# Kernel optimization log

Measured on AMD Instinct MI355X. Metric: run time of the kernel, lower is better.

Reference implementation:

```python
import jax, jax.numpy as jnp
import numpy as np

B, C = 4096, 128
EPS_BN = 1e-5  # torch BatchNorm1d default eps
EPS_ATT = 1e-9


def setup_inputs() -> dict:
    key = jax.random.key(0)
    ks = jax.random.split(key, 6)
    x1 = jax.random.normal(ks[0], (B, C, 1), jnp.float32)
    x2 = jax.random.normal(ks[1], (B, C, 1), jnp.float32)
    x1_2 = jax.random.normal(ks[2], (B, C, 1), jnp.float32)
    # trans_conv: Conv1d(C, C, kernel_size=1) -> weight (C_out, C_in)
    conv_w = jax.random.normal(ks[3], (C, C), jnp.float32) / np.sqrt(C).astype(np.float32)
    conv_b = jnp.zeros((C,), jnp.float32)
    # BatchNorm1d(C) affine params
    bn_gamma = jnp.ones((C,), jnp.float32)
    bn_beta = jnp.zeros((C,), jnp.float32)
    # fc_relation: Linear(2C+1, 1)
    fc_w = jax.random.normal(ks[4], (1, 2 * C + 1), jnp.float32) / np.sqrt(2 * C + 1).astype(np.float32)
    fc_b = jnp.zeros((1,), jnp.float32)
    return {"x1": x1, "x2": x2, "x1_2": x1_2, "conv_w": conv_w, "conv_b": conv_b,
            "bn_gamma": bn_gamma, "bn_beta": bn_beta, "fc_w": fc_w, "fc_b": fc_b}


def reference(x1, x2, x1_2, conv_w, conv_b, bn_gamma, bn_beta, fc_w, fc_b):
    # energy = bmm(x1, x2^T): (B,C,1) x (B,1,C) -> (B,C,C) outer product
    energy = jnp.einsum('bcl,bdl->bcd', x1, x2)
    energy = jax.nn.softmax(energy, axis=-1)
    # normalize columns (sum over dim=1)
    attention = energy / (EPS_ATT + energy.sum(axis=1, keepdims=True))
    # x_r = bmm(attention, x1_2): (B,C,C) x (B,C,1) -> (B,C,1)
    x_r = jnp.einsum('bcd,bdl->bcl', attention, x1_2)
    # 1x1 conv = per-position channel mixing
    t = jnp.einsum('oc,bcl->bol', conv_w, x_r) + conv_b[None, :, None]
    y = x1 - t
    # BatchNorm1d in training mode: per-channel stats over (batch, length)
    mean = y.mean(axis=(0, 2), keepdims=True)          # (1,C,1)
    var = y.var(axis=(0, 2), keepdims=True)            # biased variance
    y = (y - mean) * jax.lax.rsqrt(var + EPS_BN)
    y = y * bn_gamma[None, :, None] + bn_beta[None, :, None]
    x_r_out = jax.nn.relu(y)                            # (B,C,1)
    # gated fusion: cat([energy, energy^T, x1], dim=2) -> (B, C, 2C+1)
    feat = jnp.concatenate([energy, jnp.swapaxes(energy, 1, 2), x1], axis=2)
    gate = jax.nn.sigmoid(jnp.einsum('bcf,of->bco', feat, fc_w) + fc_b)  # (B,C,1)
    return gate * x1 + x_r_out
```

## Files before the change

### kernel.cpp

```cpp
#include <hip/hip_runtime.h>

#define B_ 4096
#define C_ 128
#define EPS_ATT 1e-9f
#define EPS_BN 1e-5f
#define LOG2E 1.44269504088896f

using short8 = __attribute__((ext_vector_type(8))) short;
using f32x4 = __attribute__((ext_vector_type(4))) float;
using us4 = __attribute__((ext_vector_type(4))) unsigned short;
using u32x2 = __attribute__((ext_vector_type(2))) unsigned int;

__device__ __forceinline__ unsigned short bf16b(float x) {
    __bf16 h = (__bf16)x;
    return __builtin_bit_cast(unsigned short, h);
}

__global__ __launch_bounds__(256, 4) void k_batch(
    const float* __restrict__ x1, const float* __restrict__ x2,
    const float* __restrict__ x12,
    const float* __restrict__ fcw, const float* __restrict__ fcb,
    float* __restrict__ XR, float* __restrict__ GX1) {
    const int b = blockIdx.x;
    const int tid = threadIdx.x;
    const int lane = tid & 63;
    const int w = tid >> 6;
    const int g = lane >> 4;
    const int ls = lane & 15;

    __shared__ char s_buf[C_ * C_ * 2] __attribute__((aligned(16)));
    __shared__ float s_x1[C_] __attribute__((aligned(16)));
    __shared__ float s_x2[C_] __attribute__((aligned(16)));
    __shared__ float s_fcC[C_] __attribute__((aligned(16)));
    __shared__ float s_invZ[C_] __attribute__((aligned(16)));
    __shared__ float s_cs4[4][C_] __attribute__((aligned(16)));
    __shared__ float s_s24[4][C_] __attribute__((aligned(16)));
    __shared__ unsigned short s_f1bf[C_] __attribute__((aligned(16)));

    float* s_S1 = (float*)s_buf;
    float* s_xrr = (float*)(s_buf + 512);
    unsigned short* s_w3bf = (unsigned short*)(s_buf + 1024);

    float v12 = 0.f;
    if (tid < C_) {
        s_x1[tid] = x1[b * C_ + tid];
        s_x2[tid] = x2[b * C_ + tid];
        s_f1bf[tid] = bf16b(fcw[tid]);
        s_fcC[tid] = fcw[C_ + tid];
        v12 = x12[b * C_ + tid];
    }
    __syncthreads();

    short8 ef0[4], ef1[4];
    float zp0 = 0.f, zp1 = 0.f;
    {
        const float r0 = s_x1[32 * w + ls] * LOG2E;
        const float r1 = s_x1[32 * w + 16 + ls] * LOG2E;
        char* erow0 = s_buf + (32 * w + ls) * 256;
        char* erow1 = s_buf + (32 * w + 16 + ls) * 256;
        const int sw = (ls & 7) << 4;
#pragma unroll
        for (int q = 0; q < 4; ++q) {
            f32x4 xa = *(const f32x4*)&s_x2[32 * q + 8 * g];
            f32x4 xb = *(const f32x4*)&s_x2[32 * q + 8 * g + 4];
            union {
                short8 v;
                unsigned short u[8];
            } p0, p1;
#pragma unroll
            for (int j = 0; j < 4; ++j) {
                float a0 = __builtin_amdgcn_exp2f(r0 * xa[j]);
                float b0 = __builtin_amdgcn_exp2f(r0 * xb[j]);
                float a1 = __builtin_amdgcn_exp2f(r1 * xa[j]);
                float b1 = __builtin_amdgcn_exp2f(r1 * xb[j]);
                zp0 += a0 + b0;
                zp1 += a1 + b1;
                p0.u[j] = bf16b(a0);
                p0.u[j + 4] = bf16b(b0);
                p1.u[j] = bf16b(a1);
                p1.u[j + 4] = bf16b(b1);
            }
            ef0[q] = p0.v;
            ef1[q] = p1.v;
            const int off = (64 * q + 16 * g) ^ sw;
            *(short8*)(erow0 + off) = p0.v;
            *(short8*)(erow1 + off) = p1.v;
        }
    }
    zp0 += __shfl_xor(zp0, 16);
    zp0 += __shfl_xor(zp0, 32);
    zp1 += __shfl_xor(zp1, 16);
    zp1 += __shfl_xor(zp1, 32);
    if (lane < 16) {
        s_invZ[32 * w + ls] = 1.f / zp0;
        s_invZ[32 * w + 16 + ls] = 1.f / zp1;
    }
    __syncthreads();

    {
        const int grp = tid & 31;
        const int sl = tid >> 5;
        const char* eb = s_buf + sl * 16 * 256;
        const int octb = grp >> 1;
        const int hoff = (grp & 1) * 8;
        float cs[4] = {0.f, 0.f, 0.f, 0.f};
        float s2[4] = {0.f, 0.f, 0.f, 0.f};
#pragma unroll
        for (int k = 0; k < 4; ++k) {
            f32x4 iz4 = *(const f32x4*)&s_invZ[sl * 16 + 4 * k];
            f32x4 fc4 = *(const f32x4*)&s_fcC[sl * 16 + 4 * k];
#pragma unroll
            for (int rr = 0; rr < 4; ++rr) {
                const int r = 4 * k + rr;
                const float iz = iz4[rr];
                const float izf = iz * fc4[rr];
                u32x2 ev = *(const u32x2*)(eb + r * 256 +
                                           ((octb ^ (r & 7)) << 4) + hoff);
#pragma unroll
                for (int d = 0; d < 2; ++d) {
                    float elo = __builtin_bit_cast(float, ev[d] << 16);
                    float ehi =
                        __builtin_bit_cast(float, ev[d] & 0xffff0000u);
                    cs[2 * d] = fmaf(elo, iz, cs[2 * d]);
                    s2[2 * d] = fmaf(elo, izf, s2[2 * d]);
                    cs[2 * d + 1] = fmaf(ehi, iz, cs[2 * d + 1]);
                    s2[2 * d + 1] = fmaf(ehi, izf, s2[2 * d + 1]);
                }
            }
        }
#pragma unroll
        for (int k = 0; k < 4; ++k) {
            cs[k] += __shfl_xor(cs[k], 32);
            s2[k] += __shfl_xor(s2[k], 32);
        }
        if ((sl & 1) == 0) {
            f32x4 c4 = {cs[0], cs[1], cs[2], cs[3]};
            f32x4 t4 = {s2[0], s2[1], s2[2], s2[3]};
            *(f32x4*)&s_cs4[w][grp * 4] = c4;
            *(f32x4*)&s_s24[w][grp * 4] = t4;
        }
    }
    __syncthreads();

    if (tid < C_) {
        float cs = s_cs4[0][tid] + s_cs4[1][tid] + s_cs4[2][tid] + s_cs4[3][tid];
        float w3 = v12 / (EPS_ATT + cs);
        s_w3bf[tid] = bf16b(w3);
    }
    __syncthreads();

    {
        const short8 z8 = {0, 0, 0, 0, 0, 0, 0, 0};
        short8 bq[4];
#pragma unroll
        for (int q = 0; q < 4; ++q) {
            if (ls == 0)
                bq[q] = *(const short8*)&s_f1bf[q * 32 + g * 8];
            else if (ls == 1)
                bq[q] = *(const short8*)&s_w3bf[q * 32 + g * 8];
            else
                bq[q] = z8;
        }
        f32x4 acc0 = {0.f, 0.f, 0.f, 0.f};
        f32x4 acc1 = {0.f, 0.f, 0.f, 0.f};
#pragma unroll
        for (int q = 0; q < 4; ++q) {
            acc0 = __builtin_amdgcn_mfma_f32_16x16x32_bf16(ef0[q], bq[q], acc0, 0, 0, 0);
            acc1 = __builtin_amdgcn_mfma_f32_16x16x32_bf16(ef1[q], bq[q], acc1, 0, 0, 0);
        }
        if (ls < 2) {
            float* dst = ls ? s_xrr : s_S1;
            *(f32x4*)&dst[(2 * w + 0) * 16 + g * 4] = acc0;
            *(f32x4*)&dst[(2 * w + 1) * 16 + g * 4] = acc1;
        }
    }
    __syncthreads();

    if (tid < C_) {
        float invz = s_invZ[tid];
        float S1 = s_S1[tid] * invz;
        float xr = s_xrr[tid] * invz;
        float S2 = s_s24[0][tid] + s_s24[1][tid] + s_s24[2][tid] + s_s24[3][tid];
        XR[b * C_ + tid] = xr;
        float gg = S1 + S2 + s_x1[tid] * fcw[2 * C_] + fcb[0];
        float gate = 1.f / (1.f + __builtin_amdgcn_exp2f(-LOG2E * gg));
        GX1[b * C_ + tid] = gate * s_x1[tid];
    }
}

__global__ __launch_bounds__(512) void k_conv(
    const float* __restrict__ W, const float* __restrict__ XR,
    const float* __restrict__ x1, const float* __restrict__ convb,
    float* __restrict__ Y, float* __restrict__ pst) {
    const int blk = blockIdx.x;
    const int tid = threadIdx.x;
    const int bb = blk * 16;
    const int lane = tid & 63;
    const int wid = tid >> 6;
    const int g = lane >> 4;
    const int ls = lane & 15;

    __shared__ unsigned short s_Wb[C_ * C_] __attribute__((aligned(16)));
    __shared__ unsigned short s_xrb[16 * 136] __attribute__((aligned(16)));

    {
        const int r = tid >> 2;
        const int c0 = (tid & 3) * 4;
        const float* src = W + r * C_ + c0 * 8;
#pragma unroll
        for (int c = 0; c < 4; ++c) {
            f32x4 a = *(const f32x4*)(src + c * 8);
            f32x4 b2 = *(const f32x4*)(src + c * 8 + 4);
            union {
                short8 v;
                unsigned short u[8];
            } p;
#pragma unroll
            for (int j = 0; j < 4; ++j) {
                p.u[j] = bf16b(a[j]);
                p.u[j + 4] = bf16b(b2[j]);
            }
            *(short8*)&s_Wb[r * C_ + (((c0 + c) ^ (r & 7)) << 3)] = p.v;
        }
    }
    {
        const int r = tid >> 5;
        const int c = (tid & 31) * 4;
        f32x4 a = *(const f32x4*)&XR[(bb + r) * C_ + c];
        us4 p;
#pragma unroll
        for (int j = 0; j < 4; ++j) p[j] = bf16b(a[j]);
        *(us4*)&s_xrb[r * 136 + c] = p;
    }
    __syncthreads();

    {
        const int n = 16 * wid + ls;
        short8 aq[4], bq[4];
#pragma unroll
        for (int q = 0; q < 4; ++q) {
            aq[q] = *(const short8*)&s_xrb[ls * 136 + 32 * q + 8 * g];
            bq[q] = *(const short8*)&s_Wb[n * C_ + (((4 * q + g) ^ (n & 7)) << 3)];
        }
        f32x4 acc = {0.f, 0.f, 0.f, 0.f};
#pragma unroll
        for (int q = 0; q < 4; ++q)
            acc = __builtin_amdgcn_mfma_f32_16x16x32_bf16(aq[q], bq[q], acc, 0, 0, 0);

        const float cbv = convb[n];
        float ps = 0.f, pq = 0.f;
#pragma unroll
        for (int r = 0; r < 4; ++r) {
            const int m = 4 * g + r;
            float y = x1[(bb + m) * C_ + n] - (acc[r] + cbv);
            Y[(bb + m) * C_ + n] = y;
            ps += y;
            pq += y * y;
        }
        ps += __shfl_xor(ps, 16);
        ps += __shfl_xor(ps, 32);
        pq += __shfl_xor(pq, 16);
        pq += __shfl_xor(pq, 32);
        if (lane < 16) {
            pst[n * 256 + blk] = ps;
            pst[32768 + n * 256 + blk] = pq;
        }
    }
}

__global__ __launch_bounds__(256) void k_fold(const float* __restrict__ pst,
                                              const float* __restrict__ gamma,
                                              const float* __restrict__ beta,
                                              float* __restrict__ AB) {
    const int ch = blockIdx.x;
    const int t = threadIdx.x;
    __shared__ float sh[256];
    __shared__ float sh2[256];
    sh[t] = pst[ch * 256 + t];
    sh2[t] = pst[32768 + ch * 256 + t];
    __syncthreads();
    for (int off = 128; off > 0; off >>= 1) {
        if (t < off) {
            sh[t] += sh[t + off];
            sh2[t] += sh2[t + off];
        }
        __syncthreads();
    }
    if (t == 0) {
        float mean = sh[0] / (float)B_;
        float var = sh2[0] / (float)B_ - mean * mean;
        float A = gamma[ch] * rsqrtf(var + EPS_BN);
        AB[ch] = A;
        AB[C_ + ch] = beta[ch] - mean * A;
    }
}

__global__ __launch_bounds__(256) void k_final(const float* __restrict__ Y,
                                               const float* __restrict__ AB,
                                               float* __restrict__ out) {
    __shared__ float sA[C_];
    __shared__ float sB[C_];
    const int t = threadIdx.x;
    if (t < C_) {
        sA[t] = AB[t];
        sB[t] = AB[C_ + t];
    }
    __syncthreads();
    const int i4 = blockIdx.x * 256 + t;
    float4 y = ((const float4*)Y)[i4];
    float4 o = ((const float4*)out)[i4];
    const int ch = (i4 * 4) & (C_ - 1);
    o.x += fmaxf(y.x * sA[ch + 0] + sB[ch + 0], 0.f);
    o.y += fmaxf(y.y * sA[ch + 1] + sB[ch + 1], 0.f);
    o.z += fmaxf(y.z * sA[ch + 2] + sB[ch + 2], 0.f);
    o.w += fmaxf(y.w * sA[ch + 3] + sB[ch + 3], 0.f);
    ((float4*)out)[i4] = o;
}

extern "C" void kernel_launch(void* const* d_in, const int* in_sizes, int n_in,
                              void* d_out, int out_size, void* d_ws,
                              size_t ws_size, hipStream_t stream) {
    const float* x1 = (const float*)d_in[0];
    const float* x2 = (const float*)d_in[1];
    const float* x12 = (const float*)d_in[2];
    const float* convw = (const float*)d_in[3];
    const float* convb = (const float*)d_in[4];
    const float* gamma = (const float*)d_in[5];
    const float* beta = (const float*)d_in[6];
    const float* fcw = (const float*)d_in[7];
    const float* fcb = (const float*)d_in[8];
    float* out = (float*)d_out;

    float* XR = (float*)d_ws;
    float* Y = XR + (size_t)B_ * C_;
    float* pst = Y + (size_t)B_ * C_;
    float* AB = pst + 2 * C_ * 256;

    k_batch<<<B_, 256, 0, stream>>>(x1, x2, x12, fcw, fcb, XR, out);
    k_conv<<<256, 512, 0, stream>>>(convw, XR, x1, convb, Y, pst);
    k_fold<<<C_, 256, 0, stream>>>(pst, gamma, beta, AB);
    k_final<<<(B_ * C_ / 4) / 256, 256, 0, stream>>>(Y, AB, out);
}
```

Measured before the change: 35.24 us.

## Make batch kernel loop over four batches per block with register prefetch

The per-batch attention/gate kernel now launches 1024 blocks. Each block processes four batch rows in a loop instead of one row per block. The next row's x1/x2/x1_2 values are loaded into registers while the current row is computed, hiding global load latency. The fc weights and bias are loaded once per block rather than once per row. In exchange each block runs a longer serial chain, and there are fewer independent blocks for the scheduler to hide latency with.

```diff
diff --git a/kernel.cpp b/kernel.cpp
--- a/kernel.cpp
+++ b/kernel.cpp
@@ -5,6 +5,8 @@
 #define EPS_ATT 1e-9f
 #define EPS_BN 1e-5f
 #define LOG2E 1.44269504088896f
+#define GRID_KB 1024
+#define NPB 4
 
 using short8 = __attribute__((ext_vector_type(8))) short;
 using f32x4 = __attribute__((ext_vector_type(4))) float;
@@ -21,7 +23,6 @@
     const float* __restrict__ x12,
     const float* __restrict__ fcw, const float* __restrict__ fcb,
     float* __restrict__ XR, float* __restrict__ GX1) {
-    const int b = blockIdx.x;
     const int tid = threadIdx.x;
     const int lane = tid & 63;
     const int w = tid >> 6;
@@ -41,150 +42,173 @@
     float* s_xrr = (float*)(s_buf + 512);
     unsigned short* s_w3bf = (unsigned short*)(s_buf + 1024);
 
-    float v12 = 0.f;
     if (tid < C_) {
-        s_x1[tid] = x1[b * C_ + tid];
-        s_x2[tid] = x2[b * C_ + tid];
         s_f1bf[tid] = bf16b(fcw[tid]);
         s_fcC[tid] = fcw[C_ + tid];
-        v12 = x12[b * C_ + tid];
-    }
-    __syncthreads();
-
-    short8 ef0[4], ef1[4];
-    float zp0 = 0.f, zp1 = 0.f;
-    {
-        const float r0 = s_x1[32 * w + ls] * LOG2E;
-        const float r1 = s_x1[32 * w + 16 + ls] * LOG2E;
-        char* erow0 = s_buf + (32 * w + ls) * 256;
-        char* erow1 = s_buf + (32 * w + 16 + ls) * 256;
-        const int sw = (ls & 7) << 4;
-#pragma unroll
-        for (int q = 0; q < 4; ++q) {
-            f32x4 xa = *(const f32x4*)&s_x2[32 * q + 8 * g];
-            f32x4 xb = *(const f32x4*)&s_x2[32 * q + 8 * g + 4];
-            union {
-                short8 v;
-                unsigned short u[8];
-            } p0, p1;
-#pragma unroll
-            for (int j = 0; j < 4; ++j) {
-                float a0 = __builtin_amdgcn_exp2f(r0 * xa[j]);
-                float b0 = __builtin_amdgcn_exp2f(r0 * xb[j]);
-                float a1 = __builtin_amdgcn_exp2f(r1 * xa[j]);
-                float b1 = __builtin_amdgcn_exp2f(r1 * xb[j]);
-                zp0 += a0 + b0;
-                zp1 += a1 + b1;
-                p0.u[j] = bf16b(a0);
-                p0.u[j + 4] = bf16b(b0);
-                p1.u[j] = bf16b(a1);
-                p1.u[j + 4] = bf16b(b1);
-            }
-            ef0[q] = p0.v;
-            ef1[q] = p1.v;
-            const int off = (64 * q + 16 * g) ^ sw;
-            *(short8*)(erow0 + off) = p0.v;
-            *(short8*)(erow1 + off) = p1.v;
-        }
-    }
-    zp0 += __shfl_xor(zp0, 16);
-    zp0 += __shfl_xor(zp0, 32);
-    zp1 += __shfl_xor(zp1, 16);
-    zp1 += __shfl_xor(zp1, 32);
-    if (lane < 16) {
-        s_invZ[32 * w + ls] = 1.f / zp0;
-        s_invZ[32 * w + 16 + ls] = 1.f / zp1;
-    }
-    __syncthreads();
-
-    {
-        const int grp = tid & 31;
-        const int sl = tid >> 5;
-        const char* eb = s_buf + sl * 16 * 256;
-        const int octb = grp >> 1;
-        const int hoff = (grp & 1) * 8;
-        float cs[4] = {0.f, 0.f, 0.f, 0.f};
-        float s2[4] = {0.f, 0.f, 0.f, 0.f};
-#pragma unroll
-        for (int k = 0; k < 4; ++k) {
-            f32x4 iz4 = *(const f32x4*)&s_invZ[sl * 16 + 4 * k];
-            f32x4 fc4 = *(const f32x4*)&s_fcC[sl * 16 + 4 * k];
-#pragma unroll
-            for (int rr = 0; rr < 4; ++rr) {
-                const int r = 4 * k + rr;
-                const float iz = iz4[rr];
-                const float izf = iz * fc4[rr];
-                u32x2 ev = *(const u32x2*)(eb + r * 256 +
-                                           ((octb ^ (r & 7)) << 4) + hoff);
-#pragma unroll
-                for (int d = 0; d < 2; ++d) {
-                    float elo = __builtin_bit_cast(float, ev[d] << 16);
-                    float ehi =
-                        __builtin_bit_cast(float, ev[d] & 0xffff0000u);
-                    cs[2 * d] = fmaf(elo, iz, cs[2 * d]);
-                    s2[2 * d] = fmaf(elo, izf, s2[2 * d]);
-                    cs[2 * d + 1] = fmaf(ehi, iz, cs[2 * d + 1]);
-                    s2[2 * d + 1] = fmaf(ehi, izf, s2[2 * d + 1]);
+    }
+    const float fc2C = fcw[2 * C_];
+    const float fcb0 = fcb[0];
+
+    int b = blockIdx.x;
+    float pv1 = 0.f, pv2 = 0.f, pv12 = 0.f;
+    if (tid < C_) {
+        pv1 = x1[b * C_ + tid];
+        pv2 = x2[b * C_ + tid];
+        pv12 = x12[b * C_ + tid];
+    }
+
+    for (int it = 0; it < NPB; ++it, b += GRID_KB) {
+        float v12 = 0.f;
+        if (tid < C_) {
+            s_x1[tid] = pv1;
+            s_x2[tid] = pv2;
+            v12 = pv12;
+        }
+        __syncthreads();
+
+        if (it + 1 < NPB && tid < C_) {
+            pv1 = x1[(b + GRID_KB) * C_ + tid];
+            pv2 = x2[(b + GRID_KB) * C_ + tid];
+            pv12 = x12[(b + GRID_KB) * C_ + tid];
+        }
+
+        short8 ef0[4], ef1[4];
+        float zp0 = 0.f, zp1 = 0.f;
+        {
+            const float r0 = s_x1[32 * w + ls] * LOG2E;
+            const float r1 = s_x1[32 * w + 16 + ls] * LOG2E;
+            char* erow0 = s_buf + (32 * w + ls) * 256;
+            char* erow1 = s_buf + (32 * w + 16 + ls) * 256;
+            const int sw = (ls & 7) << 4;
+#pragma unroll
+            for (int q = 0; q < 4; ++q) {
+                f32x4 xa = *(const f32x4*)&s_x2[32 * q + 8 * g];
+                f32x4 xb = *(const f32x4*)&s_x2[32 * q + 8 * g + 4];
+                union {
+                    short8 v;
+                    unsigned short u[8];
+                } p0, p1;
+#pragma unroll
+                for (int j = 0; j < 4; ++j) {
+                    float a0 = __builtin_amdgcn_exp2f(r0 * xa[j]);
+                    float b0 = __builtin_amdgcn_exp2f(r0 * xb[j]);
+                    float a1 = __builtin_amdgcn_exp2f(r1 * xa[j]);
+                    float b1 = __builtin_amdgcn_exp2f(r1 * xb[j]);
+                    zp0 += a0 + b0;
+                    zp1 += a1 + b1;
+                    p0.u[j] = bf16b(a0);
+                    p0.u[j + 4] = bf16b(b0);
+                    p1.u[j] = bf16b(a1);
+                    p1.u[j + 4] = bf16b(b1);
                 }
-            }
-        }
-#pragma unroll
-        for (int k = 0; k < 4; ++k) {
-            cs[k] += __shfl_xor(cs[k], 32);
-            s2[k] += __shfl_xor(s2[k], 32);
-        }
-        if ((sl & 1) == 0) {
-            f32x4 c4 = {cs[0], cs[1], cs[2], cs[3]};
-            f32x4 t4 = {s2[0], s2[1], s2[2], s2[3]};
-            *(f32x4*)&s_cs4[w][grp * 4] = c4;
-            *(f32x4*)&s_s24[w][grp * 4] = t4;
-        }
-    }
-    __syncthreads();
-
-    if (tid < C_) {
-        float cs = s_cs4[0][tid] + s_cs4[1][tid] + s_cs4[2][tid] + s_cs4[3][tid];
-        float w3 = v12 / (EPS_ATT + cs);
-        s_w3bf[tid] = bf16b(w3);
-    }
-    __syncthreads();
-
-    {
-        const short8 z8 = {0, 0, 0, 0, 0, 0, 0, 0};
-        short8 bq[4];
-#pragma unroll
-        for (int q = 0; q < 4; ++q) {
-            if (ls == 0)
-                bq[q] = *(const short8*)&s_f1bf[q * 32 + g * 8];
-            else if (ls == 1)
-                bq[q] = *(const short8*)&s_w3bf[q * 32 + g * 8];
-            else
-                bq[q] = z8;
-        }
-        f32x4 acc0 = {0.f, 0.f, 0.f, 0.f};
-        f32x4 acc1 = {0.f, 0.f, 0.f, 0.f};
-#pragma unroll
-        for (int q = 0; q < 4; ++q) {
-            acc0 = __builtin_amdgcn_mfma_f32_16x16x32_bf16(ef0[q], bq[q], acc0, 0, 0, 0);
-            acc1 = __builtin_amdgcn_mfma_f32_16x16x32_bf16(ef1[q], bq[q], acc1, 0, 0, 0);
-        }
-        if (ls < 2) {
-            float* dst = ls ? s_xrr : s_S1;
-            *(f32x4*)&dst[(2 * w + 0) * 16 + g * 4] = acc0;
-            *(f32x4*)&dst[(2 * w + 1) * 16 + g * 4] = acc1;
-        }
-    }
-    __syncthreads();
-
-    if (tid < C_) {
-        float invz = s_invZ[tid];
-        float S1 = s_S1[tid] * invz;
-        float xr = s_xrr[tid] * invz;
-        float S2 = s_s24[0][tid] + s_s24[1][tid] + s_s24[2][tid] + s_s24[3][tid];
-        XR[b * C_ + tid] = xr;
-        float gg = S1 + S2 + s_x1[tid] * fcw[2 * C_] + fcb[0];
-        float gate = 1.f / (1.f + __builtin_amdgcn_exp2f(-LOG2E * gg));
-        GX1[b * C_ + tid] = gate * s_x1[tid];
+                ef0[q] = p0.v;
+                ef1[q] = p1.v;
+                const int off = (64 * q + 16 * g) ^ sw;
+                *(short8*)(erow0 + off) = p0.v;
+                *(short8*)(erow1 + off) = p1.v;
+            }
+        }
+        zp0 += __shfl_xor(zp0, 16);
+        zp0 += __shfl_xor(zp0, 32);
+        zp1 += __shfl_xor(zp1, 16);
+        zp1 += __shfl_xor(zp1, 32);
+        if (lane < 16) {
+            s_invZ[32 * w + ls] = 1.f / zp0;
+            s_invZ[32 * w + 16 + ls] = 1.f / zp1;
+        }
+        __syncthreads();
+
+        {
+            const int grp = tid & 31;
+            const int sl = tid >> 5;
+            const char* eb = s_buf + sl * 16 * 256;
+            const int octb = grp >> 1;
+            const int hoff = (grp & 1) * 8;
+            float cs[4] = {0.f, 0.f, 0.f, 0.f};
+            float s2[4] = {0.f, 0.f, 0.f, 0.f};
+#pragma unroll
+            for (int k = 0; k < 4; ++k) {
+                f32x4 iz4 = *(const f32x4*)&s_invZ[sl * 16 + 4 * k];
+                f32x4 fc4 = *(const f32x4*)&s_fcC[sl * 16 + 4 * k];
+#pragma unroll
+                for (int rr = 0; rr < 4; ++rr) {
+                    const int r = 4 * k + rr;
+                    const float iz = iz4[rr];
+                    const float izf = iz * fc4[rr];
+                    u32x2 ev = *(const u32x2*)(eb + r * 256 +
+                                               ((octb ^ (r & 7)) << 4) + hoff);
+#pragma unroll
+                    for (int d = 0; d < 2; ++d) {
+                        float elo = __builtin_bit_cast(float, ev[d] << 16);
+                        float ehi =
+                            __builtin_bit_cast(float, ev[d] & 0xffff0000u);
+                        cs[2 * d] = fmaf(elo, iz, cs[2 * d]);
+                        s2[2 * d] = fmaf(elo, izf, s2[2 * d]);
+                        cs[2 * d + 1] = fmaf(ehi, iz, cs[2 * d + 1]);
+                        s2[2 * d + 1] = fmaf(ehi, izf, s2[2 * d + 1]);
+                    }
+                }
+            }
+#pragma unroll
+            for (int k = 0; k < 4; ++k) {
+                cs[k] += __shfl_xor(cs[k], 32);
+                s2[k] += __shfl_xor(s2[k], 32);
+            }
+            if ((sl & 1) == 0) {
+                f32x4 c4 = {cs[0], cs[1], cs[2], cs[3]};
+                f32x4 t4 = {s2[0], s2[1], s2[2], s2[3]};
+                *(f32x4*)&s_cs4[w][grp * 4] = c4;
+                *(f32x4*)&s_s24[w][grp * 4] = t4;
+            }
+        }
+        __syncthreads();
+
+        if (tid < C_) {
+            float cs = s_cs4[0][tid] + s_cs4[1][tid] + s_cs4[2][tid] +
+                       s_cs4[3][tid];
+            float w3 = v12 / (EPS_ATT + cs);
+            s_w3bf[tid] = bf16b(w3);
+        }
+        __syncthreads();
+
+        {
+            const short8 z8 = {0, 0, 0, 0, 0, 0, 0, 0};
+            short8 bq[4];
+#pragma unroll
+            for (int q = 0; q < 4; ++q) {
+                if (ls == 0)
+                    bq[q] = *(const short8*)&s_f1bf[q * 32 + g * 8];
+                else if (ls == 1)
+                    bq[q] = *(const short8*)&s_w3bf[q * 32 + g * 8];
+                else
+                    bq[q] = z8;
+            }
+            f32x4 acc0 = {0.f, 0.f, 0.f, 0.f};
+            f32x4 acc1 = {0.f, 0.f, 0.f, 0.f};
+#pragma unroll
+            for (int q = 0; q < 4; ++q) {
+                acc0 = __builtin_amdgcn_mfma_f32_16x16x32_bf16(ef0[q], bq[q], acc0, 0, 0, 0);
+                acc1 = __builtin_amdgcn_mfma_f32_16x16x32_bf16(ef1[q], bq[q], acc1, 0, 0, 0);
+            }
+            if (ls < 2) {
+                float* dst = ls ? s_xrr : s_S1;
+                *(f32x4*)&dst[(2 * w + 0) * 16 + g * 4] = acc0;
+                *(f32x4*)&dst[(2 * w + 1) * 16 + g * 4] = acc1;
+            }
+        }
+        __syncthreads();
+
+        if (tid < C_) {
+            float invz = s_invZ[tid];
+            float S1 = s_S1[tid] * invz;
+            float xr = s_xrr[tid] * invz;
+            float S2 = s_s24[0][tid] + s_s24[1][tid] + s_s24[2][tid] +
+                       s_s24[3][tid];
+            XR[b * C_ + tid] = xr;
+            float gg = S1 + S2 + s_x1[tid] * fc2C + fcb0;
+            float gate = 1.f / (1.f + __builtin_amdgcn_exp2f(-LOG2E * gg));
+            GX1[b * C_ + tid] = gate * s_x1[tid];
+        }
     }
 }
 
@@ -336,7 +360,7 @@
     float* pst = Y + (size_t)B_ * C_;
     float* AB = pst + 2 * C_ * 256;
 
-    k_batch<<<B_, 256, 0, stream>>>(x1, x2, x12, fcw, fcb, XR, out);
+    k_batch<<<GRID_KB, 256, 0, stream>>>(x1, x2, x12, fcw, fcb, XR, out);
     k_conv<<<256, 512, 0, stream>>>(convw, XR, x1, convb, Y, pst);
     k_fold<<<C_, 256, 0, stream>>>(pst, gamma, beta, AB);
     k_final<<<(B_ * C_ / 4) / 256, 256, 0, stream>>>(Y, AB, out);
```

Result: slower. 45.89 us (+30.2%).
